# Performance work log

Measured on AMD Instinct MI355X. Metric: run time of the kernel, lower is better.

Reference implementation:

```python
import jax, jax.numpy as jnp
import numpy as np

B, T, D = 4, 2048, 512
H, DK = 4, 16
MU = 1.0


def _xavier(key, shape):
    lim = float(np.sqrt(6.0 / (shape[0] + shape[1])))
    return jax.random.uniform(key, shape, jnp.float32, -lim, lim)


def setup_inputs() -> dict:
    key = jax.random.key(0)
    ks = jax.random.split(key, 9)
    x = jax.random.normal(ks[0], (B, T, D), jnp.float32)
    Wq = _xavier(ks[1], (D, H * DK))
    Wk = _xavier(ks[2], (D, H * DK))
    Wv = _xavier(ks[3], (D, H * DK))
    # W_a is zero-initialized in the module; use small random values so the
    # decay path is exercised non-trivially.
    Wa = 0.02 * jax.random.normal(ks[4], (D, H), jnp.float32)
    ba = 0.02 * jax.random.normal(ks[5], (H,), jnp.float32)
    Wg = 0.02 * jax.random.normal(ks[6], (D, H * DK), jnp.float32)
    bg = jnp.zeros((H * DK,), jnp.float32)
    Wo = _xavier(ks[7], (H * DK, D))
    return {"x": x, "Wq": Wq, "Wk": Wk, "Wv": Wv, "Wa": Wa, "ba": ba,
            "Wg": Wg, "bg": bg, "Wo": Wo}


def reference(x, Wq, Wk, Wv, Wa, ba, Wg, bg, Wo):
    b_, t_, _ = x.shape
    q = (x @ Wq).reshape(b_, t_, H, DK)
    k = (x @ Wk).reshape(b_, t_, H, DK)
    v = (x @ Wv).reshape(b_, t_, H, DK)
    # bid b_s = <q_s, k_s>/sqrt(dk); decay a_s = -softplus(x W_a + c_a) <= 0
    bid = jnp.sum(q * k, axis=-1) / np.sqrt(DK)      # (B, T, H)
    a = -jax.nn.softplus(x @ Wa + ba)                # (B, T, H)
    # Closed form of the sequential scan:
    #   scores[t, s] = bid[s] + sum_{r=s+1..t} a[r] = (bid[s] - cumA[s]) + cumA[t]
    # Row-constant cumA[t] cancels in the softmax, so the attention weights are
    # a causal softmax over mu * (bid[s] - cumA[s]).
    cumA = jnp.cumsum(a, axis=1)                     # (B, T, H)
    lg = (bid - cumA).transpose(0, 2, 1)             # (B, H, S_keys)
    mask = jnp.tril(jnp.ones((t_, t_), bool))        # keys s <= query t
    scores = jnp.where(mask[None, None], MU * lg[:, :, None, :], -jnp.inf)
    w = jax.nn.softmax(scores, axis=-1)              # (B, H, T, S)
    y = jnp.einsum('bhts,bshd->bthd', w, v)          # (B, T, H, DK)
    gate = jax.nn.sigmoid(x @ Wg + bg).reshape(b_, t_, H, DK)
    y = (y * gate).reshape(b_, t_, H * DK)
    return y @ Wo
```

## Files before the change

kernel.cpp:

```cpp
#include <hip/hip_runtime.h>
#include <math.h>

#define B_    4
#define T_    2048
#define D_    512
#define H_    4
#define ROWS_ 8192
#define CHSZ_ 128
#define NCHK_ 16

typedef unsigned short ushort_t;
typedef unsigned int   uint_t;
typedef __attribute__((ext_vector_type(8))) __bf16         bfx8;
typedef __attribute__((ext_vector_type(8))) unsigned short u16x8;
typedef __attribute__((ext_vector_type(4))) float          fx4;

__device__ __forceinline__ ushort_t f2bf(float f) {
    union { float f; uint_t u; } v; v.f = f;
    return (ushort_t)((v.u + 0x7FFFu + ((v.u >> 16) & 1u)) >> 16);
}
__device__ __forceinline__ float bf2f(ushort_t u) {
    union { uint_t u; float f; } v; v.u = ((uint_t)u) << 16; return v.f;
}

__global__ __launch_bounds__(256) void pack_w(const float* __restrict__ Wq,
                                              const float* __restrict__ Wk,
                                              const float* __restrict__ Wv,
                                              const float* __restrict__ Wg,
                                              const float* __restrict__ Wo,
                                              ushort_t* __restrict__ WcatT2,
                                              ushort_t* __restrict__ WoT) {
    int idx = blockIdx.x * 256 + threadIdx.x;
    if (idx < 256 * 512) {
        int n = idx >> 9, d = idx & 511;
        int h = n >> 6, r = n & 63, part = r >> 4, j = r & 15;
        int col = h * 16 + j;
        const float* W = (part == 0) ? Wq : (part == 1) ? Wk : (part == 2) ? Wv : Wg;
        WcatT2[idx] = f2bf(W[(size_t)d * 64 + col]);
    } else {
        int r = idx - 256 * 512;
        int n = r >> 6, k = r & 63;
        WoT[r] = f2bf(Wo[(size_t)k * 512 + n]);
    }
}

__global__ __launch_bounds__(256) void gemm_scanA(const float* __restrict__ x,
                                                  const float* __restrict__ Wa,
                                                  const float* __restrict__ ba,
                                                  const ushort_t* __restrict__ WcatT2,
                                                  float* __restrict__ stateWS,
                                                  float* __restrict__ chunkSum,
                                                  ushort_t* __restrict__ gBuf) {
    __shared__ ushort_t As[128 * 72];
    __shared__ ushort_t Bs[64 * 72];
    __shared__ float s_wa[512];
    __shared__ float s_a[128];
    __shared__ float s_a0;
    __shared__ float s_wmax[2];
    __shared__ float s_tot[17];

    const int rc = blockIdx.x & 63;
    const int h  = blockIdx.x >> 6;
    const int m0 = rc * 128;
    const int n0 = h * 64;
    const int b  = rc >> 4, chunk = rc & 15;
    const int bh = b * 4 + h;

    const int tid = threadIdx.x;
    const int wave = tid >> 6, lane = tid & 63;
    const int fr = lane & 15, quad = lane >> 4;
    const int sr = tid >> 3, sc = (tid & 7) * 8;

    s_wa[tid * 2]     = Wa[(size_t)(tid * 2) * 4 + h];
    s_wa[tid * 2 + 1] = Wa[(size_t)(tid * 2 + 1) * 4 + h];

    fx4 acc[2][4];
    #pragma unroll
    for (int i = 0; i < 2; i++)
        #pragma unroll
        for (int j = 0; j < 4; j++) acc[i][j] = (fx4)0.f;

    float pa[4] = {0.f, 0.f, 0.f, 0.f};

    float4 raF[4][2];
    u16x8  rb[2];
    #pragma unroll
    for (int s = 0; s < 4; s++) {
        const float* xp = x + (size_t)(m0 + s * 32 + sr) * D_ + sc;
        raF[s][0] = *(const float4*)xp;
        raF[s][1] = *(const float4*)(xp + 4);
    }
    #pragma unroll
    for (int s = 0; s < 2; s++)
        rb[s] = *(const u16x8*)(WcatT2 + (size_t)(n0 + s * 32 + sr) * D_ + sc);

    __syncthreads();

    for (int it = 0; it < 8; it++) {
        const int kb = it * 64 + sc;
        #pragma unroll
        for (int s = 0; s < 4; s++) {
            float xv[8] = {raF[s][0].x, raF[s][0].y, raF[s][0].z, raF[s][0].w,
                           raF[s][1].x, raF[s][1].y, raF[s][1].z, raF[s][1].w};
            u16x8 u;
            #pragma unroll
            for (int j = 0; j < 8; j++) {
                u[j] = f2bf(xv[j]);
                pa[s] = fmaf(xv[j], s_wa[kb + j], pa[s]);
            }
            *(u16x8*)&As[(s * 32 + sr) * 72 + sc] = u;
        }
        #pragma unroll
        for (int s = 0; s < 2; s++)
            *(u16x8*)&Bs[(s * 32 + sr) * 72 + sc] = rb[s];
        __syncthreads();
        if (it < 7) {
            const int k0 = (it + 1) * 64;
            #pragma unroll
            for (int s = 0; s < 4; s++) {
                const float* xp = x + (size_t)(m0 + s * 32 + sr) * D_ + k0 + sc;
                raF[s][0] = *(const float4*)xp;
                raF[s][1] = *(const float4*)(xp + 4);
            }
            #pragma unroll
            for (int s = 0; s < 2; s++)
                rb[s] = *(const u16x8*)(WcatT2 + (size_t)(n0 + s * 32 + sr) * D_ + k0 + sc);
        }
        #pragma unroll
        for (int ks = 0; ks < 64; ks += 32) {
            bfx8 af[2], bfr[4];
            #pragma unroll
            for (int mi = 0; mi < 2; mi++)
                af[mi] = *(const bfx8*)&As[(wave * 32 + mi * 16 + fr) * 72 + ks + quad * 8];
            #pragma unroll
            for (int ni = 0; ni < 4; ni++)
                bfr[ni] = *(const bfx8*)&Bs[(ni * 16 + fr) * 72 + ks + quad * 8];
            #pragma unroll
            for (int mi = 0; mi < 2; mi++)
                #pragma unroll
                for (int ni = 0; ni < 4; ni++)
                    acc[mi][ni] = __builtin_amdgcn_mfma_f32_16x16x32_bf16(af[mi], bfr[ni], acc[mi][ni], 0, 0, 0);
        }
        __syncthreads();
    }

    #pragma unroll
    for (int mi = 0; mi < 2; mi++)
        #pragma unroll
        for (int ni = 0; ni < 4; ni++)
            #pragma unroll
            for (int r = 0; r < 4; r++) {
                int rl = wave * 32 + mi * 16 + quad * 4 + r;
                int cl = ni * 16 + fr;
                As[rl * 72 + cl] = f2bf(acc[mi][ni][r]);
            }

    #pragma unroll
    for (int s = 0; s < 4; s++) {
        #pragma unroll
        for (int m = 1; m < 8; m <<= 1) pa[s] += __shfl_xor(pa[s], m, 8);
    }
    if ((tid & 7) == 0) {
        const float bah = ba[h];
        #pragma unroll
        for (int s = 0; s < 4; s++) {
            float z = pa[s] + bah;
            s_a[s * 32 + sr] = -(fmaxf(z, 0.f) + log1pf(expf(-fabsf(z))));
        }
    }
    __syncthreads();

    const bool active = (tid < 128);
    float bid = 0.f, a = 0.f;
    float v[16];
    if (active) {
        const ushort_t* ct = &As[tid * 72];
        u16x8 q0 = *(const u16x8*)(ct +  0), q1 = *(const u16x8*)(ct +  8);
        u16x8 k0 = *(const u16x8*)(ct + 16), k1 = *(const u16x8*)(ct + 24);
        u16x8 v0 = *(const u16x8*)(ct + 32), v1 = *(const u16x8*)(ct + 40);
        #pragma unroll
        for (int j = 0; j < 8; j++) {
            bid = fmaf(bf2f(q0[j]), bf2f(k0[j]), bid);
            bid = fmaf(bf2f(q1[j]), bf2f(k1[j]), bid);
            v[j]     = bf2f(v0[j]);
            v[8 + j] = bf2f(v1[j]);
        }
        bid *= 0.25f;
        a = s_a[tid];
    }

    float ca = a;
    #pragma unroll
    for (int off = 1; off < 64; off <<= 1) {
        float up = __shfl_up(ca, off);
        if (lane >= off) ca += up;
    }
    if (tid == 63) s_a0 = ca;
    __syncthreads();
    if (active && wave == 1) ca += s_a0;

    float lg = bid - ca;

    float Mw = active ? lg : -1e30f;
    #pragma unroll
    for (int off = 32; off; off >>= 1) Mw = fmaxf(Mw, __shfl_xor(Mw, off));
    if (active && lane == 0) s_wmax[wave] = Mw;
    __syncthreads();
    const float M0 = s_wmax[0], M1 = s_wmax[1];
    const float Mc = fmaxf(M0, M1);

    float d = active ? __expf(lg - Mw) : 0.f;
    float n[16];
    #pragma unroll
    for (int j = 0; j < 16; j++) n[j] = d * v[j];
    #pragma unroll
    for (int off = 1; off < 64; off <<= 1) {
        float ud = __shfl_up(d, off);
        float un[16];
        #pragma unroll
        for (int j = 0; j < 16; j++) un[j] = __shfl_up(n[j], off);
        if (lane >= off) {
            d += ud;
            #pragma unroll
            for (int j = 0; j < 16; j++) n[j] += un[j];
        }
    }
    if (tid == 63) {
        s_tot[0] = d;
        #pragma unroll
        for (int j = 0; j < 16; j++) s_tot[1 + j] = n[j];
    }
    __syncthreads();
    if (active && wave == 1) {
        float al = __expf(M0 - Mc), be = __expf(M1 - Mc);
        d = s_tot[0] * al + d * be;
        #pragma unroll
        for (int j = 0; j < 16; j++) n[j] = s_tot[1 + j] * al + n[j] * be;
    }
    const float myM = (wave == 0) ? M0 : Mc;

    if (active) {
        const int t = chunk * CHSZ_ + tid;
        const size_t eidx = (size_t)bh * T_ + t;
        stateWS[eidx] = myM;
        stateWS[32768 + eidx] = d;
        #pragma unroll
        for (int j = 0; j < 16; j++) stateWS[(size_t)(2 + j) * 32768 + eidx] = n[j];

        const ushort_t* ct = &As[tid * 72];
        u16x8 g0 = *(const u16x8*)(ct + 48), g1 = *(const u16x8*)(ct + 56);
        *(u16x8*)(gBuf + eidx * 16)     = g0;
        *(u16x8*)(gBuf + eidx * 16 + 8) = g1;

        if (tid == 127) {
            float* cs = chunkSum + (size_t)(bh * NCHK_ + chunk) * 20;
            cs[0] = Mc; cs[1] = d;
            #pragma unroll
            for (int j = 0; j < 16; j++) cs[2 + j] = n[j];
            cs[18] = ca;
        }
    }
}

__global__ __launch_bounds__(256) void scan_gemm(const float* __restrict__ stateWS,
                                                 const float* __restrict__ chunkSum,
                                                 const ushort_t* __restrict__ gBuf,
                                                 const float* __restrict__ bg,
                                                 const ushort_t* __restrict__ WoT,
                                                 float* __restrict__ C) {
    __shared__ ushort_t Ys[64 * 72];
    __shared__ ushort_t Bs[128 * 72];
    __shared__ float s_pref[4][18];

    const int m0 = blockIdx.y * 64;
    const int n0 = blockIdx.x * 128;
    const int b  = m0 >> 11;
    const int tt = m0 & 2047;
    const int chunk = tt >> 7;

    const int tid = threadIdx.x;
    const int wave = tid >> 6, lane = tid & 63;

    const int sr = tid >> 3, sc = (tid & 7) * 8;
    #pragma unroll
    for (int s = 0; s < 4; s++) {
        int rr = s * 32 + sr;
        *(u16x8*)&Bs[rr * 72 + sc] = *(const u16x8*)(WoT + (size_t)(n0 + rr) * 64 + sc);
    }

    const int h = wave, r = lane;
    const int bh = b * 4 + h;
    const size_t eidx = (size_t)bh * T_ + tt + r;
    float m_row = stateWS[eidx];
    float d_row = stateWS[32768 + eidx];
    float n_row[16];
    #pragma unroll
    for (int j = 0; j < 16; j++) n_row[j] = stateWS[(size_t)(2 + j) * 32768 + eidx];
    u16x8 g0 = *(const u16x8*)(gBuf + eidx * 16);
    u16x8 g1 = *(const u16x8*)(gBuf + eidx * 16 + 8);

    if (wave == 0) {
        const int hh = lane >> 4, p = lane & 15;
        const int bhh = b * 4 + hh;
        float mf = -1e30f, dd = 0.f, aT = 0.f;
        float nn[16];
        #pragma unroll
        for (int j = 0; j < 16; j++) nn[j] = 0.f;
        if (p < chunk) {
            const float* cs = chunkSum + (size_t)(bhh * NCHK_ + p) * 20;
            mf = cs[0]; dd = cs[1];
            #pragma unroll
            for (int j = 0; j < 16; j++) nn[j] = cs[2 + j];
            aT = cs[18];
        }
        float off = aT;
        #pragma unroll
        for (int s = 1; s < 16; s <<= 1) {
            float t2 = __shfl_down(off, s, 16);
            if (p + s < chunk) off += t2;
        }
        if (p < chunk) mf += off;
        #pragma unroll
        for (int s = 1; s < 16; s <<= 1) {
            float m2 = __shfl_xor(mf, s, 16);
            float d2 = __shfl_xor(dd, s, 16);
            float mx = fmaxf(mf, m2);
            float al = __expf(mf - mx), be = __expf(m2 - mx);
            #pragma unroll
            for (int j = 0; j < 16; j++) {
                float n2 = __shfl_xor(nn[j], s, 16);
                nn[j] = nn[j] * al + n2 * be;
            }
            dd = dd * al + d2 * be;
            mf = mx;
        }
        if (p == 0) {
            s_pref[hh][0] = mf; s_pref[hh][1] = dd;
            #pragma unroll
            for (int j = 0; j < 16; j++) s_pref[hh][2 + j] = nn[j];
        }
    }
    __syncthreads();

    {
        const float M = s_pref[h][0], D = s_pref[h][1];
        const float mx = fmaxf(M, m_row);
        const float al = __expf(M - mx), be = __expf(m_row - mx);
        const float invd = 1.f / (D * al + d_row * be);
        u16x8 o0, o1;
        #pragma unroll
        for (int j = 0; j < 16; j++) {
            float Nj = s_pref[h][2 + j] * al + n_row[j] * be;
            float gpre = ((j < 8) ? bf2f(g0[j]) : bf2f(g1[j - 8])) + bg[h * 16 + j];
            float gate = 1.f / (1.f + __expf(-gpre));
            ushort_t yb = f2bf(Nj * invd * gate);
            if (j < 8) o0[j] = yb; else o1[j - 8] = yb;
        }
        *(u16x8*)&Ys[r * 72 + h * 16]     = o0;
        *(u16x8*)&Ys[r * 72 + h * 16 + 8] = o1;
    }
    __syncthreads();

    const int wr = wave >> 1, wc = wave & 1;
    const int fr = lane & 15, quad = lane >> 4;
    fx4 acc[2][4];
    #pragma unroll
    for (int i = 0; i < 2; i++)
        #pragma unroll
        for (int j = 0; j < 4; j++) acc[i][j] = (fx4)0.f;

    #pragma unroll
    for (int ks = 0; ks < 64; ks += 32) {
        bfx8 af[2], bfr[4];
        #pragma unroll
        for (int mi = 0; mi < 2; mi++)
            af[mi] = *(const bfx8*)&Ys[(wr * 32 + mi * 16 + fr) * 72 + ks + quad * 8];
        #pragma unroll
        for (int ni = 0; ni < 4; ni++)
            bfr[ni] = *(const bfx8*)&Bs[(wc * 64 + ni * 16 + fr) * 72 + ks + quad * 8];
        #pragma unroll
        for (int mi = 0; mi < 2; mi++)
            #pragma unroll
            for (int ni = 0; ni < 4; ni++)
                acc[mi][ni] = __builtin_amdgcn_mfma_f32_16x16x32_bf16(af[mi], bfr[ni], acc[mi][ni], 0, 0, 0);
    }

    #pragma unroll
    for (int mi = 0; mi < 2; mi++)
        #pragma unroll
        for (int ni = 0; ni < 4; ni++)
            #pragma unroll
            for (int rr = 0; rr < 4; rr++) {
                int orow = m0 + wr * 32 + mi * 16 + quad * 4 + rr;
                int ocol = n0 + wc * 64 + ni * 16 + fr;
                C[(size_t)orow * D_ + ocol] = acc[mi][ni][rr];
            }
}

extern "C" void kernel_launch(void* const* d_in, const int* in_sizes, int n_in,
                              void* d_out, int out_size, void* d_ws, size_t ws_size,
                              hipStream_t stream) {
    const float* x  = (const float*)d_in[0];
    const float* Wq = (const float*)d_in[1];
    const float* Wk = (const float*)d_in[2];
    const float* Wv = (const float*)d_in[3];
    const float* Wa = (const float*)d_in[4];
    const float* ba = (const float*)d_in[5];
    const float* Wg = (const float*)d_in[6];
    const float* bg = (const float*)d_in[7];
    const float* Wo = (const float*)d_in[8];
    float* out = (float*)d_out;

    char* w = (char*)d_ws;
    ushort_t* WcatT2   = (ushort_t*)w;  w += 256 * 512 * 2;
    ushort_t* WoT      = (ushort_t*)w;  w += 512 * 64 * 2;
    float*    stateWS  = (float*)w;     w += (size_t)18 * 32768 * 4;
    float*    chunkSum = (float*)w;     w += 256 * 20 * 4;
    ushort_t* gBuf     = (ushort_t*)w;  w += (size_t)32768 * 16 * 2;

    pack_w<<<640, 256, 0, stream>>>(Wq, Wk, Wv, Wg, Wo, WcatT2, WoT);
    gemm_scanA<<<256, 256, 0, stream>>>(x, Wa, ba, WcatT2,
                                        stateWS, chunkSum, gBuf);
    scan_gemm<<<dim3(4, 128), 256, 0, stream>>>(stateWS, chunkSum, gBuf, bg, WoT, out);
}
```

Baseline: 103.6 us.

## Halve scan chunk size to 64 rows, doubling gemm_scanA grid

Shrinks each chunk handled by gemm_scanA from 128 to 64 rows, launching 512 blocks instead of 256. Each block now does a single-wave intra-chunk scan, with no cross-wave combine or the extra barriers it needed. The cross-chunk prefix in scan_gemm now combines 32 chunk summaries per head using two waves. The aim is more parallelism across the GPU. In exchange, each block rereads the same weight tile for fewer rows, three of the four waves sit idle during the scan phase, and the prefix combine is longer.

```diff
diff --git a/kernel.cpp b/kernel.cpp
--- a/kernel.cpp
+++ b/kernel.cpp
@@ -6,8 +6,8 @@
 #define D_    512
 #define H_    4
 #define ROWS_ 8192
-#define CHSZ_ 128
-#define NCHK_ 16
+#define CHSZ_ 64
+#define NCHK_ 32
 
 typedef unsigned short ushort_t;
 typedef unsigned int   uint_t;
@@ -51,19 +51,16 @@
                                                   float* __restrict__ stateWS,
                                                   float* __restrict__ chunkSum,
                                                   ushort_t* __restrict__ gBuf) {
-    __shared__ ushort_t As[128 * 72];
+    __shared__ ushort_t As[64 * 72];
     __shared__ ushort_t Bs[64 * 72];
     __shared__ float s_wa[512];
-    __shared__ float s_a[128];
-    __shared__ float s_a0;
-    __shared__ float s_wmax[2];
-    __shared__ float s_tot[17];
-
-    const int rc = blockIdx.x & 63;
-    const int h  = blockIdx.x >> 6;
-    const int m0 = rc * 128;
+    __shared__ float s_a[64];
+
+    const int rc = blockIdx.x & 127;
+    const int h  = blockIdx.x >> 7;
+    const int m0 = rc * 64;
     const int n0 = h * 64;
-    const int b  = rc >> 4, chunk = rc & 15;
+    const int b  = rc >> 5, chunk = rc & 31;
     const int bh = b * 4 + h;
 
     const int tid = threadIdx.x;
@@ -74,32 +71,28 @@
     s_wa[tid * 2]     = Wa[(size_t)(tid * 2) * 4 + h];
     s_wa[tid * 2 + 1] = Wa[(size_t)(tid * 2 + 1) * 4 + h];
 
-    fx4 acc[2][4];
-    #pragma unroll
-    for (int i = 0; i < 2; i++)
-        #pragma unroll
-        for (int j = 0; j < 4; j++) acc[i][j] = (fx4)0.f;
-
-    float pa[4] = {0.f, 0.f, 0.f, 0.f};
-
-    float4 raF[4][2];
+    fx4 acc[4];
+    #pragma unroll
+    for (int j = 0; j < 4; j++) acc[j] = (fx4)0.f;
+
+    float pa[2] = {0.f, 0.f};
+
+    float4 raF[2][2];
     u16x8  rb[2];
     #pragma unroll
-    for (int s = 0; s < 4; s++) {
+    for (int s = 0; s < 2; s++) {
         const float* xp = x + (size_t)(m0 + s * 32 + sr) * D_ + sc;
         raF[s][0] = *(const float4*)xp;
         raF[s][1] = *(const float4*)(xp + 4);
-    }
-    #pragma unroll
-    for (int s = 0; s < 2; s++)
         rb[s] = *(const u16x8*)(WcatT2 + (size_t)(n0 + s * 32 + sr) * D_ + sc);
+    }
 
     __syncthreads();
 
     for (int it = 0; it < 8; it++) {
         const int kb = it * 64 + sc;
         #pragma unroll
-        for (int s = 0; s < 4; s++) {
+        for (int s = 0; s < 2; s++) {
             float xv[8] = {raF[s][0].x, raF[s][0].y, raF[s][0].z, raF[s][0].w,
                            raF[s][1].x, raF[s][1].y, raF[s][1].z, raF[s][1].w};
             u16x8 u;
@@ -109,75 +102,62 @@
                 pa[s] = fmaf(xv[j], s_wa[kb + j], pa[s]);
             }
             *(u16x8*)&As[(s * 32 + sr) * 72 + sc] = u;
-        }
-        #pragma unroll
-        for (int s = 0; s < 2; s++)
             *(u16x8*)&Bs[(s * 32 + sr) * 72 + sc] = rb[s];
+        }
         __syncthreads();
         if (it < 7) {
             const int k0 = (it + 1) * 64;
             #pragma unroll
-            for (int s = 0; s < 4; s++) {
+            for (int s = 0; s < 2; s++) {
                 const float* xp = x + (size_t)(m0 + s * 32 + sr) * D_ + k0 + sc;
                 raF[s][0] = *(const float4*)xp;
                 raF[s][1] = *(const float4*)(xp + 4);
-            }
-            #pragma unroll
-            for (int s = 0; s < 2; s++)
                 rb[s] = *(const u16x8*)(WcatT2 + (size_t)(n0 + s * 32 + sr) * D_ + k0 + sc);
+            }
         }
         #pragma unroll
         for (int ks = 0; ks < 64; ks += 32) {
-            bfx8 af[2], bfr[4];
-            #pragma unroll
-            for (int mi = 0; mi < 2; mi++)
-                af[mi] = *(const bfx8*)&As[(wave * 32 + mi * 16 + fr) * 72 + ks + quad * 8];
-            #pragma unroll
-            for (int ni = 0; ni < 4; ni++)
-                bfr[ni] = *(const bfx8*)&Bs[(ni * 16 + fr) * 72 + ks + quad * 8];
-            #pragma unroll
-            for (int mi = 0; mi < 2; mi++)
-                #pragma unroll
-                for (int ni = 0; ni < 4; ni++)
-                    acc[mi][ni] = __builtin_amdgcn_mfma_f32_16x16x32_bf16(af[mi], bfr[ni], acc[mi][ni], 0, 0, 0);
+            bfx8 af = *(const bfx8*)&As[(wave * 16 + fr) * 72 + ks + quad * 8];
+            #pragma unroll
+            for (int ni = 0; ni < 4; ni++) {
+                bfx8 bfr = *(const bfx8*)&Bs[(ni * 16 + fr) * 72 + ks + quad * 8];
+                acc[ni] = __builtin_amdgcn_mfma_f32_16x16x32_bf16(af, bfr, acc[ni], 0, 0, 0);
+            }
         }
         __syncthreads();
     }
 
     #pragma unroll
-    for (int mi = 0; mi < 2; mi++)
-        #pragma unroll
-        for (int ni = 0; ni < 4; ni++)
-            #pragma unroll
-            for (int r = 0; r < 4; r++) {
-                int rl = wave * 32 + mi * 16 + quad * 4 + r;
-                int cl = ni * 16 + fr;
-                As[rl * 72 + cl] = f2bf(acc[mi][ni][r]);
-            }
-
-    #pragma unroll
-    for (int s = 0; s < 4; s++) {
+    for (int ni = 0; ni < 4; ni++)
+        #pragma unroll
+        for (int r = 0; r < 4; r++) {
+            int rl = wave * 16 + quad * 4 + r;
+            int cl = ni * 16 + fr;
+            As[rl * 72 + cl] = f2bf(acc[ni][r]);
+        }
+
+    #pragma unroll
+    for (int s = 0; s < 2; s++) {
         #pragma unroll
         for (int m = 1; m < 8; m <<= 1) pa[s] += __shfl_xor(pa[s], m, 8);
     }
     if ((tid & 7) == 0) {
         const float bah = ba[h];
         #pragma unroll
-        for (int s = 0; s < 4; s++) {
+        for (int s = 0; s < 2; s++) {
             float z = pa[s] + bah;
             s_a[s * 32 + sr] = -(fmaxf(z, 0.f) + log1pf(expf(-fabsf(z))));
         }
     }
     __syncthreads();
 
-    const bool active = (tid < 128);
-    float bid = 0.f, a = 0.f;
-    float v[16];
-    if (active) {
-        const ushort_t* ct = &As[tid * 72];
+    if (wave == 0) {
+        const ushort_t* ct = &As[lane * 72];
         u16x8 q0 = *(const u16x8*)(ct +  0), q1 = *(const u16x8*)(ct +  8);
         u16x8 k0 = *(const u16x8*)(ct + 16), k1 = *(const u16x8*)(ct + 24);
         u16x8 v0 = *(const u16x8*)(ct + 32), v1 = *(const u16x8*)(ct + 40);
+        float bid = 0.f;
+        float v[16];
         #pragma unroll
         for (int j = 0; j < 8; j++) {
             bid = fmaf(bf2f(q0[j]), bf2f(k0[j]), bid);
@@ -186,73 +166,50 @@
             v[8 + j] = bf2f(v1[j]);
         }
         bid *= 0.25f;
-        a = s_a[tid];
-    }
-
-    float ca = a;
-    #pragma unroll
-    for (int off = 1; off < 64; off <<= 1) {
-        float up = __shfl_up(ca, off);
-        if (lane >= off) ca += up;
-    }
-    if (tid == 63) s_a0 = ca;
-    __syncthreads();
-    if (active && wave == 1) ca += s_a0;
-
-    float lg = bid - ca;
-
-    float Mw = active ? lg : -1e30f;
-    #pragma unroll
-    for (int off = 32; off; off >>= 1) Mw = fmaxf(Mw, __shfl_xor(Mw, off));
-    if (active && lane == 0) s_wmax[wave] = Mw;
-    __syncthreads();
-    const float M0 = s_wmax[0], M1 = s_wmax[1];
-    const float Mc = fmaxf(M0, M1);
-
-    float d = active ? __expf(lg - Mw) : 0.f;
-    float n[16];
-    #pragma unroll
-    for (int j = 0; j < 16; j++) n[j] = d * v[j];
-    #pragma unroll
-    for (int off = 1; off < 64; off <<= 1) {
-        float ud = __shfl_up(d, off);
-        float un[16];
-        #pragma unroll
-        for (int j = 0; j < 16; j++) un[j] = __shfl_up(n[j], off);
-        if (lane >= off) {
-            d += ud;
-            #pragma unroll
-            for (int j = 0; j < 16; j++) n[j] += un[j];
-        }
-    }
-    if (tid == 63) {
-        s_tot[0] = d;
-        #pragma unroll
-        for (int j = 0; j < 16; j++) s_tot[1 + j] = n[j];
-    }
-    __syncthreads();
-    if (active && wave == 1) {
-        float al = __expf(M0 - Mc), be = __expf(M1 - Mc);
-        d = s_tot[0] * al + d * be;
-        #pragma unroll
-        for (int j = 0; j < 16; j++) n[j] = s_tot[1 + j] * al + n[j] * be;
-    }
-    const float myM = (wave == 0) ? M0 : Mc;
-
-    if (active) {
-        const int t = chunk * CHSZ_ + tid;
+        float a = s_a[lane];
+
+        float ca = a;
+        #pragma unroll
+        for (int off = 1; off < 64; off <<= 1) {
+            float up = __shfl_up(ca, off);
+            if (lane >= off) ca += up;
+        }
+
+        float lg = bid - ca;
+
+        float Mc = lg;
+        #pragma unroll
+        for (int off = 32; off; off >>= 1) Mc = fmaxf(Mc, __shfl_xor(Mc, off));
+
+        float d = __expf(lg - Mc);
+        float n[16];
+        #pragma unroll
+        for (int j = 0; j < 16; j++) n[j] = d * v[j];
+        #pragma unroll
+        for (int off = 1; off < 64; off <<= 1) {
+            float ud = __shfl_up(d, off);
+            float un[16];
+            #pragma unroll
+            for (int j = 0; j < 16; j++) un[j] = __shfl_up(n[j], off);
+            if (lane >= off) {
+                d += ud;
+                #pragma unroll
+                for (int j = 0; j < 16; j++) n[j] += un[j];
+            }
+        }
+
+        const int t = chunk * CHSZ_ + lane;
         const size_t eidx = (size_t)bh * T_ + t;
-        stateWS[eidx] = myM;
+        stateWS[eidx] = Mc;
         stateWS[32768 + eidx] = d;
         #pragma unroll
         for (int j = 0; j < 16; j++) stateWS[(size_t)(2 + j) * 32768 + eidx] = n[j];
 
-        const ushort_t* ct = &As[tid * 72];
         u16x8 g0 = *(const u16x8*)(ct + 48), g1 = *(const u16x8*)(ct + 56);
         *(u16x8*)(gBuf + eidx * 16)     = g0;
         *(u16x8*)(gBuf + eidx * 16 + 8) = g1;
 
-        if (tid == 127) {
+        if (lane == 63) {
             float* cs = chunkSum + (size_t)(bh * NCHK_ + chunk) * 20;
             cs[0] = Mc; cs[1] = d;
             #pragma unroll
@@ -276,7 +233,7 @@
     const int n0 = blockIdx.x * 128;
     const int b  = m0 >> 11;
     const int tt = m0 & 2047;
-    const int chunk = tt >> 7;
+    const int chunk = tt >> 6;
 
     const int tid = threadIdx.x;
     const int wave = tid >> 6, lane = tid & 63;
@@ -299,8 +256,8 @@
     u16x8 g0 = *(const u16x8*)(gBuf + eidx * 16);
     u16x8 g1 = *(const u16x8*)(gBuf + eidx * 16 + 8);
 
-    if (wave == 0) {
-        const int hh = lane >> 4, p = lane & 15;
+    if (wave < 2) {
+        const int hh = wave * 2 + (lane >> 5), p = lane & 31;
         const int bhh = b * 4 + hh;
         float mf = -1e30f, dd = 0.f, aT = 0.f;
         float nn[16];
@@ -315,20 +272,20 @@
         }
         float off = aT;
         #pragma unroll
-        for (int s = 1; s < 16; s <<= 1) {
-            float t2 = __shfl_down(off, s, 16);
+        for (int s = 1; s < 32; s <<= 1) {
+            float t2 = __shfl_down(off, s, 32);
             if (p + s < chunk) off += t2;
         }
         if (p < chunk) mf += off;
         #pragma unroll
-        for (int s = 1; s < 16; s <<= 1) {
-            float m2 = __shfl_xor(mf, s, 16);
-            float d2 = __shfl_xor(dd, s, 16);
+        for (int s = 1; s < 32; s <<= 1) {
+            float m2 = __shfl_xor(mf, s, 32);
+            float d2 = __shfl_xor(dd, s, 32);
             float mx = fmaxf(mf, m2);
             float al = __expf(mf - mx), be = __expf(m2 - mx);
             #pragma unroll
             for (int j = 0; j < 16; j++) {
-                float n2 = __shfl_xor(nn[j], s, 16);
+                float n2 = __shfl_xor(nn[j], s, 32);
                 nn[j] = nn[j] * al + n2 * be;
             }
             dd = dd * al + d2 * be;
@@ -415,11 +372,11 @@
     ushort_t* WcatT2   = (ushort_t*)w;  w += 256 * 512 * 2;
     ushort_t* WoT      = (ushort_t*)w;  w += 512 * 64 * 2;
     float*    stateWS  = (float*)w;     w += (size_t)18 * 32768 * 4;
-    float*    chunkSum = (float*)w;     w += 256 * 20 * 4;
+    float*    chunkSum = (float*)w;     w += 512 * 20 * 4;
     ushort_t* gBuf     = (ushort_t*)w;  w += (size_t)32768 * 16 * 2;
 
     pack_w<<<640, 256, 0, stream>>>(Wq, Wk, Wv, Wg, Wo, WcatT2, WoT);
-    gemm_scanA<<<256, 256, 0, stream>>>(x, Wa, ba, WcatT2,
+    gemm_scanA<<<512, 256, 0, stream>>>(x, Wa, ba, WcatT2,
                                         stateWS, chunkSum, gBuf);
     scan_gemm<<<dim3(4, 128), 256, 0, stream>>>(stateWS, chunkSum, gBuf, bg, WoT, out);
 }
```

Result: faster. 100.2 us (-3.3%).
